# Kernel tuning notes

Measured on AMD Instinct MI355X. Metric: run time of the kernel, lower is better.

The kernel has to match this reference:

```python
import jax, jax.numpy as jnp
import numpy as np

N = 50000        # nodes
E = 1600000      # edges (before self loops)
C_IN = 128
C_OUT = 128
G = 64           # graphs in the batch
NEG_SLOPE = 0.2  # GATConv default


def setup_inputs() -> dict:
    key = jax.random.key(0)
    ks = jax.random.split(key, 12)
    u = jax.random.normal(ks[0], (N, C_IN), jnp.float32)
    edge_index = jax.random.randint(ks[1], (2, E), 0, N, dtype=jnp.int32)
    batch = jnp.sort(jax.random.randint(ks[2], (N,), 0, G, dtype=jnp.int32))
    g1 = 1.0 / np.sqrt(C_IN)
    g2 = 1.0 / np.sqrt(C_OUT)
    return {
        "u": u,
        "W1": jax.random.normal(ks[3], (C_IN, C_OUT), jnp.float32) * g1,
        "a_src1": jax.random.normal(ks[4], (C_OUT,), jnp.float32) * g2,
        "a_dst1": jax.random.normal(ks[5], (C_OUT,), jnp.float32) * g2,
        "b1": jnp.zeros((C_OUT,), jnp.float32),
        "W2": jax.random.normal(ks[6], (C_OUT, C_OUT), jnp.float32) * g2,
        "a_src2": jax.random.normal(ks[7], (C_OUT,), jnp.float32) * g2,
        "a_dst2": jax.random.normal(ks[8], (C_OUT,), jnp.float32) * g2,
        "b2": jnp.zeros((C_OUT,), jnp.float32),
        "edge_index": edge_index,
        "batch": batch,
    }


def gat_conv(x, edge_index, W, a_src, a_dst, b):
    """PyG GATConv, heads=1: linear -> edge attention -> scatter softmax -> scatter add."""
    n = x.shape[0]
    h = x @ W                                        # [N, C]
    loops = jnp.arange(n, dtype=edge_index.dtype)    # add_self_loops=True
    src = jnp.concatenate([edge_index[0], loops])    # message source j
    dst = jnp.concatenate([edge_index[1], loops])    # aggregation target i
    alpha_s = h @ a_src                              # [N]
    alpha_d = h @ a_dst                              # [N]
    e = jax.nn.leaky_relu(alpha_s[src] + alpha_d[dst], NEG_SLOPE)  # [E+N]
    m = jax.ops.segment_max(e, dst, num_segments=n)  # stable softmax per target
    w = jnp.exp(e - m[dst])
    denom = jax.ops.segment_sum(w, dst, num_segments=n)
    alpha = w / denom[dst]                           # [E+N]
    out = jax.ops.segment_sum(alpha[:, None] * h[src], dst, num_segments=n)
    return out + b


def reference(u, W1, a_src1, a_dst1, b1, W2, a_src2, a_dst2, b2, edge_index, batch):
    h = jax.nn.selu(gat_conv(u, edge_index, W1, a_src1, a_dst1, b1))
    h = jax.nn.selu(gat_conv(h, edge_index, W2, a_src2, a_dst2, b2))
    # global_mean_pool
    s = jax.ops.segment_sum(h, batch, num_segments=G)                      # [G, C]
    cnt = jax.ops.segment_sum(jnp.ones((h.shape[0],), h.dtype), batch, num_segments=G)
    return s / jnp.maximum(cnt, 1.0)[:, None]
```

## Files before the change

### kernel.cpp

```cpp
#include <hip/hip_runtime.h>
#include <hip/hip_bf16.h>
#include <math.h>

#define CH 128
#define PSHIFT 9
#define PSIZE (1 << PSHIFT)
#define CHUNK 2048
#define EPT 8
#define MAXP 128
#define PCAP 24576
#define PS 8

typedef __attribute__((ext_vector_type(8))) short short8;
typedef __attribute__((ext_vector_type(4))) float f32x4;

__device__ __forceinline__ float seluf(float x) {
    const float scale = 1.0507009873554804934193349852946f;
    const float alpha = 1.6732632423543772848170429916717f;
    return x > 0.0f ? scale * x : scale * alpha * (__expf(x) - 1.0f);
}

__device__ __forceinline__ float lrelu(float x) {
    return x > 0.0f ? x : 0.2f * x;
}

__device__ __forceinline__ short bfc(float f) {
    union { __hip_bfloat16 b; short s; } u;
    u.b = __float2bfloat16(f);
    return u.s;
}

__device__ __forceinline__ unsigned pk(float lo, float hi) {
    return ((unsigned)(unsigned short)bfc(hi) << 16) | (unsigned short)bfc(lo);
}


__global__ __launch_bounds__(256) void k_part(const int* __restrict__ ei,
                                              int* __restrict__ pfill,
                                              unsigned long long* __restrict__ staged,
                                              int E, int NP) {
    __shared__ int hist[MAXP];
    __shared__ int base[MAXP];
    const int tid = threadIdx.x;
    const int j0 = blockIdx.x * CHUNK;
    for (int i = tid; i < NP; i += 256) hist[i] = 0;
    __syncthreads();
    int part[EPT], rank[EPT];
    unsigned long long rec[EPT];
#pragma unroll
    for (int e = 0; e < EPT; ++e) {
        int j = j0 + e * 256 + tid;
        part[e] = -1;
        if (j < E) {
            int s = ei[j], d = ei[E + j];
            part[e] = d >> PSHIFT;
            rec[e] = ((unsigned long long)(unsigned)d << 32) | (unsigned)s;
            rank[e] = atomicAdd(&hist[part[e]], 1);
        }
    }
    __syncthreads();
    for (int i = tid; i < NP; i += 256)
        base[i] = hist[i] ? atomicAdd(&pfill[i], hist[i]) : 0;
    __syncthreads();
#pragma unroll
    for (int e = 0; e < EPT; ++e)
        if (part[e] >= 0)
            staged[(size_t)part[e] * PCAP + base[part[e]] + rank[e]] = rec[e];
}

__global__ __launch_bounds__(128) void k_ptop(const int* __restrict__ pfill,
                                              int* __restrict__ pbase,
                                              int* __restrict__ rowptr,
                                              int n, int E, int NP) {
    __shared__ int sb[128];
    int t = threadIdx.x;
    int v = (t < NP) ? pfill[t] : 0;
    sb[t] = v;
    __syncthreads();
    for (int off = 1; off < 128; off <<= 1) {
        int u = (t >= off) ? sb[t - off] : 0;
        __syncthreads();
        sb[t] += u;
        __syncthreads();
    }
    if (t < NP) pbase[t] = sb[t] - v;
    if (t == NP - 1) {
        pbase[NP] = sb[t];
        rowptr[n] = E + n;
    }
}

__global__ __launch_bounds__(1024) void k_build(
    const unsigned long long* __restrict__ staged, const int* __restrict__ pfill,
    const int* __restrict__ pbase, int* __restrict__ rowptr, int* __restrict__ csr,
    int n) {
    const int p = blockIdx.x;
    const int d0 = p << PSHIFT;
    __shared__ int lcnt[PSIZE];
    __shared__ int lrow[PSIZE];
    __shared__ int sc[PSIZE];
    const int tid = threadIdx.x;
    if (tid < PSIZE) lcnt[tid] = 0;
    __syncthreads();
    const size_t rbeg = (size_t)p * PCAP;
    const size_t rend = rbeg + pfill[p];
    const int rb = pbase[p] + d0;
    for (size_t r = rbeg + tid; r < rend; r += 1024)
        atomicAdd(&lcnt[(int)(staged[r] >> 32) - d0], 1);
    __syncthreads();
    int myv = 0;
    if (tid < PSIZE) {
        myv = (d0 + tid < n) ? lcnt[tid] + 1 : 0;
        sc[tid] = myv;
    }
    __syncthreads();
    for (int off = 1; off < PSIZE; off <<= 1) {
        int u = 0;
        if (tid < PSIZE && tid >= off) u = sc[tid - off];
        __syncthreads();
        if (tid < PSIZE) sc[tid] += u;
        __syncthreads();
    }
    if (tid < PSIZE && d0 + tid < n) {
        int rp = rb + sc[tid] - myv;
        lrow[tid] = rp;
        rowptr[d0 + tid] = rp;
        csr[rp] = d0 + tid;
        lcnt[tid] = 0;
    }
    __syncthreads();
    for (size_t r = rbeg + tid; r < rend; r += 1024) {
        unsigned long long v = staged[r];
        int d = (int)(v >> 32), s = (int)(v & 0xffffffffu);
        int pos = lrow[d - d0] + 1 + atomicAdd(&lcnt[d - d0], 1);
        csr[pos] = s;
    }
}


template <typename T>
__global__ __launch_bounds__(256) void k_gemm3(
    const T* __restrict__ x, const float* __restrict__ W,
    const float* __restrict__ a_s, const float* __restrict__ a_d,
    __hip_bfloat16* __restrict__ hb, float* __restrict__ as_o,
    float* __restrict__ ad_o, int n) {
    __shared__ short WB[4 * 8 * 64 * 8];
    const int tid = threadIdx.x;
    for (int i = tid; i < CH * CH; i += 256) {
        int k = i >> 7, c = i & 127;
        int kb = k >> 5, kk = k & 31;
        int t = c >> 4;
        int ln = (c & 15) | ((kk >> 3) << 4);
        int j = kk & 7;
        WB[(((kb << 3) + t) << 9) + (ln << 3) + j] = bfc(W[i]);
    }
    __syncthreads();
    const int lane = tid & 63;
    const int wid = tid >> 6;
    const int l15 = lane & 15;
    const int lhi = lane >> 4;
    float asl[8], adl[8];
#pragma unroll
    for (int t = 0; t < 8; ++t) {
        asl[t] = a_s[t * 16 + l15];
        adl[t] = a_d[t * 16 + l15];
    }
#pragma unroll
    for (int s = 0; s < 2; ++s) {
        int r0 = blockIdx.x * 128 + s * 64 + wid * 16;
        if (r0 >= n) break;
        int ar = r0 + l15; if (ar >= n) ar = n - 1;
        const T* xr = x + (size_t)ar * CH + lhi * 8;
        f32x4 acc[8];
#pragma unroll
        for (int t = 0; t < 8; ++t) acc[t] = (f32x4){0.f, 0.f, 0.f, 0.f};
#pragma unroll
        for (int kb = 0; kb < 4; ++kb) {
            short8 af;
            if constexpr (sizeof(T) == 4) {
                float4 xa = *(const float4*)(xr + kb * 32);
                float4 xb = *(const float4*)(xr + kb * 32 + 4);
                af[0] = bfc(xa.x); af[1] = bfc(xa.y); af[2] = bfc(xa.z); af[3] = bfc(xa.w);
                af[4] = bfc(xb.x); af[5] = bfc(xb.y); af[6] = bfc(xb.z); af[7] = bfc(xb.w);
            } else {
                af = *(const short8*)(xr + kb * 32);
            }
#pragma unroll
            for (int t = 0; t < 8; ++t) {
                short8 bv = ((const short8*)WB)[(((kb << 3) + t) << 6) | lane];
                acc[t] = __builtin_amdgcn_mfma_f32_16x16x32_bf16(af, bv, acc[t], 0, 0, 0);
            }
        }
        float pa[4] = {0.f, 0.f, 0.f, 0.f}, pd[4] = {0.f, 0.f, 0.f, 0.f};
#pragma unroll
        for (int t = 0; t < 8; ++t) {
#pragma unroll
            for (int q = 0; q < 4; ++q) {
                int row = r0 + lhi * 4 + q;
                if (row < n)
                    hb[(size_t)row * CH + t * 16 + l15] = __float2bfloat16(acc[t][q]);
                pa[q] += acc[t][q] * asl[t];
                pd[q] += acc[t][q] * adl[t];
            }
        }
#pragma unroll
        for (int q = 0; q < 4; ++q) {
#pragma unroll
            for (int o = 1; o < 16; o <<= 1) {
                pa[q] += __shfl_xor(pa[q], o);
                pd[q] += __shfl_xor(pd[q], o);
            }
        }
        if (l15 == 0) {
#pragma unroll
            for (int q = 0; q < 4; ++q) {
                int row = r0 + lhi * 4 + q;
                if (row < n) { as_o[row] = pa[q]; ad_o[row] = pd[q]; }
            }
        }
    }
}


__global__ __launch_bounds__(256) void k_fused_agg(
    const int* __restrict__ rowptr, const int* __restrict__ csr,
    const float* __restrict__ as_v, const float* __restrict__ ad_v,
    float* __restrict__ wedge, const __hip_bfloat16* __restrict__ hb,
    const float* __restrict__ bias, __hip_bfloat16* __restrict__ out, int n) {
    int gw = (int)((blockIdx.x * (size_t)blockDim.x + threadIdx.x) >> 6);
    int lane = threadIdx.x & 63;
    if (gw >= n) return;
    int beg = rowptr[gw], end = rowptr[gw + 1];
    int deg = end - beg;
    float adi = ad_v[gw];

    const int quarter = lane >> 4;
    const int c8 = lane & 15;
    float acc[8];
#pragma unroll
    for (int k = 0; k < 8; ++k) acc[k] = 0.f;
    float inv;

    if (deg <= 64) {
        bool valid = lane < deg;
        int src = valid ? csr[beg + lane] : 0;
        float e = valid ? lrelu(as_v[src] + adi) : -1e30f;
        float m = e;
#pragma unroll
        for (int o = 32; o > 0; o >>= 1) m = fmaxf(m, __shfl_xor(m, o));
        float w = valid ? __expf(e - m) : 0.f;
        float s = w;
#pragma unroll
        for (int o = 32; o > 0; o >>= 1) s += __shfl_xor(s, o);
        inv = 1.0f / s;
        for (int b = 0; b < deg; b += 4) {
            int idx = b + quarter;
            float wv = __shfl(w, idx);
            int sv = __shfl(src, idx);
            uint4 hv = ((const uint4*)hb)[(size_t)sv * 16 + c8];
            acc[0] += wv * __uint_as_float(hv.x << 16);
            acc[1] += wv * __uint_as_float(hv.x & 0xffff0000u);
            acc[2] += wv * __uint_as_float(hv.y << 16);
            acc[3] += wv * __uint_as_float(hv.y & 0xffff0000u);
            acc[4] += wv * __uint_as_float(hv.z << 16);
            acc[5] += wv * __uint_as_float(hv.z & 0xffff0000u);
            acc[6] += wv * __uint_as_float(hv.w << 16);
            acc[7] += wv * __uint_as_float(hv.w & 0xffff0000u);
        }
    } else {
        float m = -1e30f;
        for (int p = beg + lane; p < end; p += 64) {
            float e = lrelu(as_v[csr[p]] + adi);
            wedge[p] = e;
            m = fmaxf(m, e);
        }
#pragma unroll
        for (int o = 32; o > 0; o >>= 1) m = fmaxf(m, __shfl_xor(m, o));
        float s = 0.f;
        for (int p = beg + lane; p < end; p += 64) {
            float wv = __expf(wedge[p] - m);
            wedge[p] = wv;
            s += wv;
        }
#pragma unroll
        for (int o = 32; o > 0; o >>= 1) s += __shfl_xor(s, o);
        inv = 1.0f / s;
        for (int p = beg; p < end; p += 4) {
            int pp = p + quarter;
            float wv; int sv;
            if (pp < end) { wv = wedge[pp]; sv = csr[pp]; }
            else { wv = 0.f; sv = 0; }
            uint4 hv = ((const uint4*)hb)[(size_t)sv * 16 + c8];
            acc[0] += wv * __uint_as_float(hv.x << 16);
            acc[1] += wv * __uint_as_float(hv.x & 0xffff0000u);
            acc[2] += wv * __uint_as_float(hv.y << 16);
            acc[3] += wv * __uint_as_float(hv.y & 0xffff0000u);
            acc[4] += wv * __uint_as_float(hv.z << 16);
            acc[5] += wv * __uint_as_float(hv.z & 0xffff0000u);
            acc[6] += wv * __uint_as_float(hv.w << 16);
            acc[7] += wv * __uint_as_float(hv.w & 0xffff0000u);
        }
    }
#pragma unroll
    for (int k = 0; k < 8; ++k) {
        acc[k] += __shfl_xor(acc[k], 16);
        acc[k] += __shfl_xor(acc[k], 32);
    }
    if (quarter == 0) {
        const float4 bv0 = ((const float4*)bias)[c8 * 2];
        const float4 bv1 = ((const float4*)bias)[c8 * 2 + 1];
        float o0 = seluf(acc[0] * inv + bv0.x);
        float o1 = seluf(acc[1] * inv + bv0.y);
        float o2 = seluf(acc[2] * inv + bv0.z);
        float o3 = seluf(acc[3] * inv + bv0.w);
        float o4 = seluf(acc[4] * inv + bv1.x);
        float o5 = seluf(acc[5] * inv + bv1.y);
        float o6 = seluf(acc[6] * inv + bv1.z);
        float o7 = seluf(acc[7] * inv + bv1.w);
        uint4 ov;
        ov.x = pk(o0, o1);
        ov.y = pk(o2, o3);
        ov.z = pk(o4, o5);
        ov.w = pk(o6, o7);
        ((uint4*)out)[(size_t)gw * 16 + c8] = ov;
    }
}


__device__ int lower_bound_dev(const int* a, int n, int key) {
    int lo = 0, hi = n;
    while (lo < hi) {
        int mid = (lo + hi) >> 1;
        if (a[mid] < key) lo = mid + 1; else hi = mid;
    }
    return lo;
}

__global__ __launch_bounds__(256) void k_pool1(const __hip_bfloat16* __restrict__ x,
                                               const int* __restrict__ batchv,
                                               float* __restrict__ part, int n) {
    int g = blockIdx.x >> 3, s = blockIdx.x & (PS - 1);
    int lo = lower_bound_dev(batchv, n, g);
    int hi = lower_bound_dev(batchv, n, g + 1);
    int lane = threadIdx.x & 63, wv = threadIdx.x >> 6;
    int slot = s * 4 + wv;
    float sx0 = 0.f, sy0 = 0.f, sx1 = 0.f, sy1 = 0.f;
    int i = lo + slot;
    for (; i + 32 < hi; i += 64) {
        unsigned u0 = ((const unsigned*)x)[(size_t)i * 64 + lane];
        unsigned u1 = ((const unsigned*)x)[(size_t)(i + 32) * 64 + lane];
        sx0 += __uint_as_float(u0 << 16);
        sy0 += __uint_as_float(u0 & 0xffff0000u);
        sx1 += __uint_as_float(u1 << 16);
        sy1 += __uint_as_float(u1 & 0xffff0000u);
    }
    if (i < hi) {
        unsigned u0 = ((const unsigned*)x)[(size_t)i * 64 + lane];
        sx0 += __uint_as_float(u0 << 16);
        sy0 += __uint_as_float(u0 & 0xffff0000u);
    }
    __shared__ float2 red[4][64];
    red[wv][lane] = make_float2(sx0 + sx1, sy0 + sy1);
    __syncthreads();
    if (wv == 0) {
        float2 a = red[0][lane], b = red[1][lane], c = red[2][lane], d = red[3][lane];
        float* pp = part + ((size_t)(g * PS + s)) * CH;
        pp[2 * lane] = a.x + b.x + c.x + d.x;
        pp[2 * lane + 1] = a.y + b.y + c.y + d.y;
    }
}

__global__ __launch_bounds__(128) void k_pool2(const float* __restrict__ part,
                                               const int* __restrict__ batchv,
                                               float* __restrict__ outp, int n) {
    int g = blockIdx.x, t = threadIdx.x;
    int lo = lower_bound_dev(batchv, n, g);
    int hi = lower_bound_dev(batchv, n, g + 1);
    float v = 0.f;
#pragma unroll
    for (int s = 0; s < PS; ++s) v += part[((size_t)(g * PS + s)) * CH + t];
    int cnt = hi - lo; if (cnt < 1) cnt = 1;
    outp[(size_t)g * CH + t] = v / (float)cnt;
}


extern "C" void kernel_launch(void* const* d_in, const int* in_sizes, int n_in,
                              void* d_out, int out_size, void* d_ws, size_t ws_size,
                              hipStream_t stream) {
    const float* u   = (const float*)d_in[0];
    const float* W1  = (const float*)d_in[1];
    const float* as1 = (const float*)d_in[2];
    const float* ad1 = (const float*)d_in[3];
    const float* b1  = (const float*)d_in[4];
    const float* W2  = (const float*)d_in[5];
    const float* as2 = (const float*)d_in[6];
    const float* ad2 = (const float*)d_in[7];
    const float* b2  = (const float*)d_in[8];
    const int* ei    = (const int*)d_in[9];
    const int* batchv= (const int*)d_in[10];

    const int N = in_sizes[0] / CH;
    const int E = in_sizes[9] / 2;
    const int M = E + N;
    const int NP = (N + PSIZE - 1) >> PSHIFT;
    const int G = out_size / CH;

    char* p = (char*)d_ws;
    auto alloc = [&](size_t bytes) {
        char* r = p;
        p += (bytes + 255) & ~(size_t)255;
        return r;
    };
    int*   pfill  = (int*)alloc((size_t)NP * 4);
    size_t zbytes = (size_t)(p - (char*)d_ws);
    int*   rowptr = (int*)alloc((size_t)(N + 1) * 4);
    int*   pbase  = (int*)alloc((size_t)(NP + 1) * 4);
    int*   csr    = (int*)alloc((size_t)M * 4);
    float* wedge  = (float*)alloc((size_t)M * 4);
    float* asv    = (float*)alloc((size_t)N * 4);
    float* adv    = (float*)alloc((size_t)N * 4);
    float* ppart  = (float*)alloc((size_t)G * PS * CH * 4);
    size_t hbytes = (size_t)N * CH * 2;
    size_t sbytes = (size_t)NP * PCAP * 8;
    char*  hs     = alloc(hbytes > sbytes ? hbytes : sbytes);
    __hip_bfloat16* hbuf = (__hip_bfloat16*)hs;
    unsigned long long* staged = (unsigned long long*)hs;
    __hip_bfloat16* x2 = (__hip_bfloat16*)alloc((size_t)N * CH * 2);

    hipMemsetAsync(d_ws, 0, zbytes, stream);

    k_part<<<(E + CHUNK - 1) / CHUNK, 256, 0, stream>>>(ei, pfill, staged, E, NP);
    k_ptop<<<1, 128, 0, stream>>>(pfill, pbase, rowptr, N, E, NP);
    k_build<<<NP, 1024, 0, stream>>>(staged, pfill, pbase, rowptr, csr, N);

    const int gblocks = (N + 127) / 128;

    k_gemm3<float><<<gblocks, 256, 0, stream>>>(u, W1, as1, ad1, hbuf, asv, adv, N);
    k_fused_agg<<<(N * 64 + 255) / 256, 256, 0, stream>>>(rowptr, csr, asv, adv, wedge, hbuf, b1, x2, N);

    k_gemm3<__hip_bfloat16><<<gblocks, 256, 0, stream>>>(x2, W2, as2, ad2, hbuf, asv, adv, N);
    k_fused_agg<<<(N * 64 + 255) / 256, 256, 0, stream>>>(rowptr, csr, asv, adv, wedge, hbuf, b2, x2, N);

    k_pool1<<<G * PS, 256, 0, stream>>>(x2, batchv, ppart, N);
    k_pool2<<<G, 128, 0, stream>>>(ppart, batchv, (float*)d_out, N);
}
```

Measured before the change: 222.0 us.

## Merge CSR build and first GEMM into one heterogeneous kernel with smaller partitions

Replaces the single-block prefix kernel and the CSR build kernel with one launch. Its first NP blocks each recompute the partition prefix sum and build their partition's CSR slice, while the remaining blocks run the layer-1 MFMA GEMM with the attention dot products, so independent work overlaps and two launches disappear. Partitions shrink to 256 destinations (256 partitions, half the capacity each) to suit 256-thread blocks. The edge-weight scratch and x2 now alias the staging buffer. The aggregation accumulators become packed float2 vectors to encourage packed FMA, and each build block redundantly scans pfill in exchange.

After: 208.1 us. -6.2%, faster.

```diff
diff --git a/kernel.cpp b/kernel.cpp
--- a/kernel.cpp
+++ b/kernel.cpp
@@ -3,16 +3,17 @@
 #include <math.h>
 
 #define CH 128
-#define PSHIFT 9
+#define PSHIFT 8
 #define PSIZE (1 << PSHIFT)
 #define CHUNK 2048
 #define EPT 8
-#define MAXP 128
-#define PCAP 24576
+#define MAXP 256
+#define PCAP 12288
 #define PS 8
 
 typedef __attribute__((ext_vector_type(8))) short short8;
 typedef __attribute__((ext_vector_type(4))) float f32x4;
+typedef __attribute__((ext_vector_type(2))) float f32x2;
 
 __device__ __forceinline__ float seluf(float x) {
     const float scale = 1.0507009873554804934193349852946f;
@@ -68,72 +69,137 @@
             staged[(size_t)part[e] * PCAP + base[part[e]] + rank[e]] = rec[e];
 }
 
-__global__ __launch_bounds__(128) void k_ptop(const int* __restrict__ pfill,
-                                              int* __restrict__ pbase,
-                                              int* __restrict__ rowptr,
-                                              int n, int E, int NP) {
-    __shared__ int sb[128];
-    int t = threadIdx.x;
-    int v = (t < NP) ? pfill[t] : 0;
-    sb[t] = v;
+
+__global__ __launch_bounds__(256) void k_fat(
+    const unsigned long long* __restrict__ staged, const int* __restrict__ pfill,
+    int* __restrict__ rowptr, int* __restrict__ csr, int n, int E, int NP,
+    const float* __restrict__ x, const float* __restrict__ W,
+    const float* __restrict__ a_s, const float* __restrict__ a_d,
+    __hip_bfloat16* __restrict__ hb, float* __restrict__ as_o,
+    float* __restrict__ ad_o) {
+    __shared__ __align__(16) char sm[32768];
+    const int tid = threadIdx.x;
+
+    if ((int)blockIdx.x < NP) {
+        int* lcnt = (int*)sm;
+        int* lrow = lcnt + PSIZE;
+        int* sc   = lrow + PSIZE;
+        int* psc  = sc + PSIZE;
+        const int p = blockIdx.x;
+        const int d0 = p << PSHIFT;
+        psc[tid] = (tid < NP) ? pfill[tid] : 0;
+        lcnt[tid] = 0;
+        __syncthreads();
+        for (int off = 1; off < 256; off <<= 1) {
+            int v = (tid >= off) ? psc[tid - off] : 0;
+            __syncthreads();
+            psc[tid] += v;
+            __syncthreads();
+        }
+        const int pbase = psc[p] - pfill[p];
+        const size_t rbeg = (size_t)p * PCAP;
+        const size_t rend = rbeg + pfill[p];
+        const int rb = pbase + d0;
+        for (size_t r = rbeg + tid; r < rend; r += 256)
+            atomicAdd(&lcnt[(int)(staged[r] >> 32) - d0], 1);
+        __syncthreads();
+        int myv = (d0 + tid < n) ? lcnt[tid] + 1 : 0;
+        sc[tid] = myv;
+        __syncthreads();
+        for (int off = 1; off < 256; off <<= 1) {
+            int v = (tid >= off) ? sc[tid - off] : 0;
+            __syncthreads();
+            sc[tid] += v;
+            __syncthreads();
+        }
+        if (d0 + tid < n) {
+            int rp = rb + sc[tid] - myv;
+            lrow[tid] = rp;
+            rowptr[d0 + tid] = rp;
+            csr[rp] = d0 + tid;
+            lcnt[tid] = 0;
+        }
+        if (p == 0 && tid == 0) rowptr[n] = E + n;
+        __syncthreads();
+        for (size_t r = rbeg + tid; r < rend; r += 256) {
+            unsigned long long v = staged[r];
+            int d = (int)(v >> 32), s = (int)(v & 0xffffffffu);
+            int pos = lrow[d - d0] + 1 + atomicAdd(&lcnt[d - d0], 1);
+            csr[pos] = s;
+        }
+        return;
+    }
+
+    short* WB = (short*)sm;
+    for (int i = tid; i < CH * CH; i += 256) {
+        int k = i >> 7, c = i & 127;
+        int kb = k >> 5, kk = k & 31;
+        int t = c >> 4;
+        int ln = (c & 15) | ((kk >> 3) << 4);
+        int j = kk & 7;
+        WB[(((kb << 3) + t) << 9) + (ln << 3) + j] = bfc(W[i]);
+    }
     __syncthreads();
-    for (int off = 1; off < 128; off <<= 1) {
-        int u = (t >= off) ? sb[t - off] : 0;
-        __syncthreads();
-        sb[t] += u;
-        __syncthreads();
-    }
-    if (t < NP) pbase[t] = sb[t] - v;
-    if (t == NP - 1) {
-        pbase[NP] = sb[t];
-        rowptr[n] = E + n;
-    }
-}
-
-__global__ __launch_bounds__(1024) void k_build(
-    const unsigned long long* __restrict__ staged, const int* __restrict__ pfill,
-    const int* __restrict__ pbase, int* __restrict__ rowptr, int* __restrict__ csr,
-    int n) {
-    const int p = blockIdx.x;
-    const int d0 = p << PSHIFT;
-    __shared__ int lcnt[PSIZE];
-    __shared__ int lrow[PSIZE];
-    __shared__ int sc[PSIZE];
-    const int tid = threadIdx.x;
-    if (tid < PSIZE) lcnt[tid] = 0;
-    __syncthreads();
-    const size_t rbeg = (size_t)p * PCAP;
-    const size_t rend = rbeg + pfill[p];
-    const int rb = pbase[p] + d0;
-    for (size_t r = rbeg + tid; r < rend; r += 1024)
-        atomicAdd(&lcnt[(int)(staged[r] >> 32) - d0], 1);
-    __syncthreads();
-    int myv = 0;
-    if (tid < PSIZE) {
-        myv = (d0 + tid < n) ? lcnt[tid] + 1 : 0;
-        sc[tid] = myv;
-    }
-    __syncthreads();
-    for (int off = 1; off < PSIZE; off <<= 1) {
-        int u = 0;
-        if (tid < PSIZE && tid >= off) u = sc[tid - off];
-        __syncthreads();
-        if (tid < PSIZE) sc[tid] += u;
-        __syncthreads();
-    }
-    if (tid < PSIZE && d0 + tid < n) {
-        int rp = rb + sc[tid] - myv;
-        lrow[tid] = rp;
-        rowptr[d0 + tid] = rp;
-        csr[rp] = d0 + tid;
-        lcnt[tid] = 0;
-    }
-    __syncthreads();
-    for (size_t r = rbeg + tid; r < rend; r += 1024) {
-        unsigned long long v = staged[r];
-        int d = (int)(v >> 32), s = (int)(v & 0xffffffffu);
-        int pos = lrow[d - d0] + 1 + atomicAdd(&lcnt[d - d0], 1);
-        csr[pos] = s;
+    const int bid = blockIdx.x - NP;
+    const int lane = tid & 63;
+    const int wid = tid >> 6;
+    const int l15 = lane & 15;
+    const int lhi = lane >> 4;
+    float asl[8], adl[8];
+#pragma unroll
+    for (int t = 0; t < 8; ++t) {
+        asl[t] = a_s[t * 16 + l15];
+        adl[t] = a_d[t * 16 + l15];
+    }
+#pragma unroll
+    for (int s = 0; s < 2; ++s) {
+        int r0 = bid * 128 + s * 64 + wid * 16;
+        if (r0 >= n) break;
+        int ar = r0 + l15; if (ar >= n) ar = n - 1;
+        const float* xr = x + (size_t)ar * CH + lhi * 8;
+        f32x4 acc[8];
+#pragma unroll
+        for (int t = 0; t < 8; ++t) acc[t] = (f32x4){0.f, 0.f, 0.f, 0.f};
+#pragma unroll
+        for (int kb = 0; kb < 4; ++kb) {
+            float4 xa = *(const float4*)(xr + kb * 32);
+            float4 xb = *(const float4*)(xr + kb * 32 + 4);
+            short8 af;
+            af[0] = bfc(xa.x); af[1] = bfc(xa.y); af[2] = bfc(xa.z); af[3] = bfc(xa.w);
+            af[4] = bfc(xb.x); af[5] = bfc(xb.y); af[6] = bfc(xb.z); af[7] = bfc(xb.w);
+#pragma unroll
+            for (int t = 0; t < 8; ++t) {
+                short8 bv = ((const short8*)WB)[(((kb << 3) + t) << 6) | lane];
+                acc[t] = __builtin_amdgcn_mfma_f32_16x16x32_bf16(af, bv, acc[t], 0, 0, 0);
+            }
+        }
+        float pa[4] = {0.f, 0.f, 0.f, 0.f}, pd[4] = {0.f, 0.f, 0.f, 0.f};
+#pragma unroll
+        for (int t = 0; t < 8; ++t) {
+#pragma unroll
+            for (int q = 0; q < 4; ++q) {
+                int row = r0 + lhi * 4 + q;
+                if (row < n)
+                    hb[(size_t)row * CH + t * 16 + l15] = __float2bfloat16(acc[t][q]);
+                pa[q] += acc[t][q] * asl[t];
+                pd[q] += acc[t][q] * adl[t];
+            }
+        }
+#pragma unroll
+        for (int q = 0; q < 4; ++q) {
+#pragma unroll
+            for (int o = 1; o < 16; o <<= 1) {
+                pa[q] += __shfl_xor(pa[q], o);
+                pd[q] += __shfl_xor(pd[q], o);
+            }
+        }
+        if (l15 == 0) {
+#pragma unroll
+            for (int q = 0; q < 4; ++q) {
+                int row = r0 + lhi * 4 + q;
+                if (row < n) { as_o[row] = pa[q]; ad_o[row] = pd[q]; }
+            }
+        }
     }
 }
 
@@ -236,9 +302,9 @@
 
     const int quarter = lane >> 4;
     const int c8 = lane & 15;
-    float acc[8];
-#pragma unroll
-    for (int k = 0; k < 8; ++k) acc[k] = 0.f;
+    f32x2 acc2[4];
+#pragma unroll
+    for (int k = 0; k < 4; ++k) acc2[k] = (f32x2){0.f, 0.f};
     float inv;
 
     if (deg <= 64) {
@@ -258,14 +324,16 @@
             float wv = __shfl(w, idx);
             int sv = __shfl(src, idx);
             uint4 hv = ((const uint4*)hb)[(size_t)sv * 16 + c8];
-            acc[0] += wv * __uint_as_float(hv.x << 16);
-            acc[1] += wv * __uint_as_float(hv.x & 0xffff0000u);
-            acc[2] += wv * __uint_as_float(hv.y << 16);
-            acc[3] += wv * __uint_as_float(hv.y & 0xffff0000u);
-            acc[4] += wv * __uint_as_float(hv.z << 16);
-            acc[5] += wv * __uint_as_float(hv.z & 0xffff0000u);
-            acc[6] += wv * __uint_as_float(hv.w << 16);
-            acc[7] += wv * __uint_as_float(hv.w & 0xffff0000u);
+            f32x2 wv2 = (f32x2){wv, wv};
+            f32x2 h0, h1, h2, h3;
+            h0.x = __uint_as_float(hv.x << 16); h0.y = __uint_as_float(hv.x & 0xffff0000u);
+            h1.x = __uint_as_float(hv.y << 16); h1.y = __uint_as_float(hv.y & 0xffff0000u);
+            h2.x = __uint_as_float(hv.z << 16); h2.y = __uint_as_float(hv.z & 0xffff0000u);
+            h3.x = __uint_as_float(hv.w << 16); h3.y = __uint_as_float(hv.w & 0xffff0000u);
+            acc2[0] += wv2 * h0;
+            acc2[1] += wv2 * h1;
+            acc2[2] += wv2 * h2;
+            acc2[3] += wv2 * h3;
         }
     } else {
         float m = -1e30f;
@@ -291,32 +359,36 @@
             if (pp < end) { wv = wedge[pp]; sv = csr[pp]; }
             else { wv = 0.f; sv = 0; }
             uint4 hv = ((const uint4*)hb)[(size_t)sv * 16 + c8];
-            acc[0] += wv * __uint_as_float(hv.x << 16);
-            acc[1] += wv * __uint_as_float(hv.x & 0xffff0000u);
-            acc[2] += wv * __uint_as_float(hv.y << 16);
-            acc[3] += wv * __uint_as_float(hv.y & 0xffff0000u);
-            acc[4] += wv * __uint_as_float(hv.z << 16);
-            acc[5] += wv * __uint_as_float(hv.z & 0xffff0000u);
-            acc[6] += wv * __uint_as_float(hv.w << 16);
-            acc[7] += wv * __uint_as_float(hv.w & 0xffff0000u);
-        }
-    }
-#pragma unroll
-    for (int k = 0; k < 8; ++k) {
-        acc[k] += __shfl_xor(acc[k], 16);
-        acc[k] += __shfl_xor(acc[k], 32);
+            f32x2 wv2 = (f32x2){wv, wv};
+            f32x2 h0, h1, h2, h3;
+            h0.x = __uint_as_float(hv.x << 16); h0.y = __uint_as_float(hv.x & 0xffff0000u);
+            h1.x = __uint_as_float(hv.y << 16); h1.y = __uint_as_float(hv.y & 0xffff0000u);
+            h2.x = __uint_as_float(hv.z << 16); h2.y = __uint_as_float(hv.z & 0xffff0000u);
+            h3.x = __uint_as_float(hv.w << 16); h3.y = __uint_as_float(hv.w & 0xffff0000u);
+            acc2[0] += wv2 * h0;
+            acc2[1] += wv2 * h1;
+            acc2[2] += wv2 * h2;
+            acc2[3] += wv2 * h3;
+        }
+    }
+#pragma unroll
+    for (int k = 0; k < 4; ++k) {
+        acc2[k].x += __shfl_xor(acc2[k].x, 16);
+        acc2[k].y += __shfl_xor(acc2[k].y, 16);
+        acc2[k].x += __shfl_xor(acc2[k].x, 32);
+        acc2[k].y += __shfl_xor(acc2[k].y, 32);
     }
     if (quarter == 0) {
         const float4 bv0 = ((const float4*)bias)[c8 * 2];
         const float4 bv1 = ((const float4*)bias)[c8 * 2 + 1];
-        float o0 = seluf(acc[0] * inv + bv0.x);
-        float o1 = seluf(acc[1] * inv + bv0.y);
-        float o2 = seluf(acc[2] * inv + bv0.z);
-        float o3 = seluf(acc[3] * inv + bv0.w);
-        float o4 = seluf(acc[4] * inv + bv1.x);
-        float o5 = seluf(acc[5] * inv + bv1.y);
-        float o6 = seluf(acc[6] * inv + bv1.z);
-        float o7 = seluf(acc[7] * inv + bv1.w);
+        float o0 = seluf(acc2[0].x * inv + bv0.x);
+        float o1 = seluf(acc2[0].y * inv + bv0.y);
+        float o2 = seluf(acc2[1].x * inv + bv0.z);
+        float o3 = seluf(acc2[1].y * inv + bv0.w);
+        float o4 = seluf(acc2[2].x * inv + bv1.x);
+        float o5 = seluf(acc2[2].y * inv + bv1.y);
+        float o6 = seluf(acc2[3].x * inv + bv1.z);
+        float o7 = seluf(acc2[3].y * inv + bv1.w);
         uint4 ov;
         ov.x = pk(o0, o1);
         ov.y = pk(o2, o3);
@@ -414,28 +486,28 @@
     int*   pfill  = (int*)alloc((size_t)NP * 4);
     size_t zbytes = (size_t)(p - (char*)d_ws);
     int*   rowptr = (int*)alloc((size_t)(N + 1) * 4);
-    int*   pbase  = (int*)alloc((size_t)(NP + 1) * 4);
     int*   csr    = (int*)alloc((size_t)M * 4);
-    float* wedge  = (float*)alloc((size_t)M * 4);
     float* asv    = (float*)alloc((size_t)N * 4);
     float* adv    = (float*)alloc((size_t)N * 4);
     float* ppart  = (float*)alloc((size_t)G * PS * CH * 4);
-    size_t hbytes = (size_t)N * CH * 2;
+    __hip_bfloat16* hbuf = (__hip_bfloat16*)alloc((size_t)N * CH * 2);
+    size_t wbytes = ((size_t)M * 4 + 255) & ~(size_t)255;
+    size_t xbytes = (size_t)N * CH * 2;
     size_t sbytes = (size_t)NP * PCAP * 8;
-    char*  hs     = alloc(hbytes > sbytes ? hbytes : sbytes);
-    __hip_bfloat16* hbuf = (__hip_bfloat16*)hs;
-    unsigned long long* staged = (unsigned long long*)hs;
-    __hip_bfloat16* x2 = (__hip_bfloat16*)alloc((size_t)N * CH * 2);
+    size_t blob   = wbytes + xbytes > sbytes ? wbytes + xbytes : sbytes;
+    char*  bb     = alloc(blob);
+    unsigned long long* staged = (unsigned long long*)bb;
+    float* wedge  = (float*)bb;
+    __hip_bfloat16* x2 = (__hip_bfloat16*)(bb + wbytes);
 
     hipMemsetAsync(d_ws, 0, zbytes, stream);
 
+    const int gblocks = (N + 127) / 128;
+
     k_part<<<(E + CHUNK - 1) / CHUNK, 256, 0, stream>>>(ei, pfill, staged, E, NP);
-    k_ptop<<<1, 128, 0, stream>>>(pfill, pbase, rowptr, N, E, NP);
-    k_build<<<NP, 1024, 0, stream>>>(staged, pfill, pbase, rowptr, csr, N);
-
-    const int gblocks = (N + 127) / 128;
-
-    k_gemm3<float><<<gblocks, 256, 0, stream>>>(u, W1, as1, ad1, hbuf, asv, adv, N);
+    k_fat<<<NP + gblocks, 256, 0, stream>>>(staged, pfill, rowptr, csr, N, E, NP,
+                                            u, W1, as1, ad1, hbuf, asv, adv);
+
     k_fused_agg<<<(N * 64 + 255) / 256, 256, 0, stream>>>(rowptr, csr, asv, adv, wedge, hbuf, b1, x2, N);
 
     k_gemm3<__hip_bfloat16><<<gblocks, 256, 0, stream>>>(x2, W2, as2, ad2, hbuf, asv, adv, N);
```
